# Performance work log

Measured on AMD Instinct MI355X. Metric: run time of the kernel, lower is better.

## Reference

```python
import jax, jax.numpy as jnp
import numpy as np

NUM_GROUPS = 32
NUM_HEAD_CH = 64
EPS = 1e-5


def setup_inputs() -> dict:
    key = jax.random.key(0)
    k1, k2, k3 = jax.random.split(key, 3)
    B, C, H, W = 16, 512, 32, 32
    return {
        "x": jax.random.normal(k1, (B, C, H, W), dtype=jnp.float32),
        "norm_w": jnp.ones((C,), dtype=jnp.float32),
        "norm_b": jnp.zeros((C,), dtype=jnp.float32),
        "qkv_w": jax.random.normal(k2, (3 * C, C), dtype=jnp.float32) * 0.02,
        "qkv_b": jnp.zeros((3 * C,), dtype=jnp.float32),
        "proj_w": jax.random.normal(k3, (C, C), dtype=jnp.float32) * 0.02,
        "proj_b": jnp.zeros((C,), dtype=jnp.float32),
    }


def _group_norm(x, w, b):
    # x: [B, C, T]
    B, C, T = x.shape
    g = x.reshape(B, NUM_GROUPS, C // NUM_GROUPS, T)
    mean = g.mean(axis=(2, 3), keepdims=True)
    var = g.var(axis=(2, 3), keepdims=True)
    g = (g - mean) * jax.lax.rsqrt(var + EPS)
    return g.reshape(B, C, T) * w[None, :, None] + b[None, :, None]


def reference(x, norm_w, norm_b, qkv_w, qkv_b, proj_w, proj_b):
    B, C, Hs, Ws = x.shape
    T = Hs * Ws
    xr = x.reshape(B, C, T)
    xn = _group_norm(xr, norm_w, norm_b)
    # 1x1 conv == matmul over channel dim
    qkv = jnp.einsum('oc,bct->bot', qkv_w, xn) + qkv_b[None, :, None]  # [B, 3C, T]
    q, k, v = jnp.split(qkv, 3, axis=1)
    nH = C // NUM_HEAD_CH
    ch = NUM_HEAD_CH
    q = q.reshape(B * nH, ch, T)
    k = k.reshape(B * nH, ch, T)
    v = v.reshape(B * nH, ch, T)
    scale = 1.0 / np.sqrt(np.sqrt(ch)).astype(np.float32)
    # [BH, T, S] score matrix, softmax in float32 (matches torch .float())
    weight = jnp.einsum('bct,bcs->bts', q * scale, k * scale)
    weight = jax.nn.softmax(weight.astype(jnp.float32), axis=-1).astype(weight.dtype)
    a = jnp.einsum('bts,bcs->bct', weight, v).reshape(B, C, T)
    h = jnp.einsum('oc,bct->bot', proj_w, a) + proj_b[None, :, None]
    return (xr + h).reshape(B, C, Hs, Ws)
```

## Files before the change

### kernel.cpp

```cpp
#include <hip/hip_runtime.h>
#include <hip/hip_bf16.h>


typedef __bf16 bf16x8 __attribute__((ext_vector_type(8)));
typedef __bf16 bf16x4 __attribute__((ext_vector_type(4)));
typedef float f32x4 __attribute__((ext_vector_type(4)));

#define MFMA16(a, b, c) __builtin_amdgcn_mfma_f32_16x16x32_bf16((a), (b), (c), 0, 0, 0)

typedef const __attribute__((address_space(1))) unsigned int* gptr_t;
typedef __attribute__((address_space(3))) unsigned int* lptr_t;

__device__ __forceinline__ void gload16(const void* g, void* l) {
  __builtin_amdgcn_global_load_lds((gptr_t)g, (lptr_t)l, 16, 0, 0);
}

__global__ __launch_bounds__(256) void cvt_bf16(const float* __restrict__ src,
                                                __hip_bfloat16* __restrict__ dst,
                                                int n4) {
  int i = blockIdx.x * 256 + threadIdx.x;
  if (i >= n4) return;
  float4 v = ((const float4*)src)[i];
  union { __hip_bfloat16 h[4]; uint2 u; } pk;
  pk.h[0] = __float2bfloat16(v.x);
  pk.h[1] = __float2bfloat16(v.y);
  pk.h[2] = __float2bfloat16(v.z);
  pk.h[3] = __float2bfloat16(v.w);
  *(uint2*)(dst + (size_t)i * 4) = pk.u;
}

__global__ __launch_bounds__(256) void gn_kernel(const float* __restrict__ x,
                                                 const float* __restrict__ nw,
                                                 const float* __restrict__ nb,
                                                 __hip_bfloat16* __restrict__ xnt) {
  const int blk = blockIdx.x;
  const int bb = blk >> 5, g = blk & 31;
  const int tid = threadIdx.x;
  const float4* xg = (const float4*)(x + ((size_t)bb * 512 + g * 16) * 1024);

  float4 vals[16];
  float s = 0.f, ss = 0.f;
#pragma unroll
  for (int k = 0; k < 16; ++k) {
    float4 v = xg[tid + 256 * k];
    vals[k] = v;
    s += v.x + v.y + v.z + v.w;
    ss += v.x * v.x + v.y * v.y + v.z * v.z + v.w * v.w;
  }
#pragma unroll
  for (int off = 1; off < 64; off <<= 1) {
    s += __shfl_xor(s, off, 64);
    ss += __shfl_xor(ss, off, 64);
  }
  __shared__ float red[8];
  const int wid = tid >> 6, lane = tid & 63;
  if (lane == 0) { red[wid] = s; red[wid + 4] = ss; }
  __syncthreads();
  s = red[0] + red[1] + red[2] + red[3];
  ss = red[4] + red[5] + red[6] + red[7];
  const float mean = s * (1.f / 16384.f);
  const float var = ss * (1.f / 16384.f) - mean * mean;
  const float rstd = rsqrtf(var + 1e-5f);

  float aa[16], cc[16];
#pragma unroll
  for (int k = 0; k < 16; ++k) {
    float w = nw[g * 16 + k];
    float b = nb[g * 16 + k];
    aa[k] = rstd * w;
    cc[k] = b - mean * aa[k];
  }
#pragma unroll
  for (int j = 0; j < 4; ++j) {
    union { __hip_bfloat16 h[16]; uint4 u[2]; } row;
#pragma unroll
    for (int k = 0; k < 16; ++k) {
      float v = ((const float*)&vals[k])[j];
      row.h[k] = __float2bfloat16(v * aa[k] + cc[k]);
    }
    size_t idx = ((size_t)bb * 1024 + 4 * tid + j) * 512 + g * 16;
    *(uint4*)(xnt + idx) = row.u[0];
    *(uint4*)(xnt + idx + 8) = row.u[1];
  }
}

template <int EPI>
__global__ __launch_bounds__(256) void gemm_bt(const __hip_bfloat16* __restrict__ A,
                                               const __hip_bfloat16* __restrict__ Bt,
                                               const float* __restrict__ bias,
                                               __hip_bfloat16* __restrict__ oq,
                                               __hip_bfloat16* __restrict__ ok,
                                               __hip_bfloat16* __restrict__ ov,
                                               const float* __restrict__ xres,
                                               float* __restrict__ of) {
  __shared__ __hip_bfloat16 Alds[128 * 64];
  __shared__ __hip_bfloat16 Blds[128 * 64];
  const int tid = threadIdx.x;
  const int wid = tid >> 6, lane = tid & 63;
  const int g = lane >> 4, tl = lane & 15;
  const int wr = wid >> 1, wc = wid & 1;
  const int id = blockIdx.y * 128 + blockIdx.x;
  const int w = id >> 3;
  const int m0 = (w >> 4) * 128;
  const int n0 = (((id & 7) << 4) | (w & 15)) * 128;

  f32x4 acc[4][4];
#pragma unroll
  for (int i = 0; i < 4; ++i)
#pragma unroll
    for (int j = 0; j < 4; ++j) acc[i][j] = (f32x4){0.f, 0.f, 0.f, 0.f};

  for (int kt = 0; kt < 8; ++kt) {
    const int k0 = kt * 64;
    __syncthreads();
#pragma unroll
    for (int qq = 0; qq < 4; ++qq) {
      const int r = qq * 32 + (tid >> 3);
      const int ko = (tid & 7) * 8;
      gload16(A + (size_t)(m0 + r) * 512 + k0 + ko,
              (char*)Alds + (qq * 2048 + wid * 512) * 2);
      gload16(Bt + (size_t)(n0 + r) * 512 + k0 + ko,
              (char*)Blds + (qq * 2048 + wid * 512) * 2);
    }
    __syncthreads();
#pragma unroll
    for (int kk = 0; kk < 2; ++kk) {
      bf16x8 af[4], bfr[4];
#pragma unroll
      for (int mi = 0; mi < 4; ++mi)
        af[mi] = *(const bf16x8*)(Alds + (wr * 64 + mi * 16 + tl) * 64 + kk * 32 + g * 8);
#pragma unroll
      for (int ni = 0; ni < 4; ++ni)
        bfr[ni] = *(const bf16x8*)(Blds + (wc * 64 + ni * 16 + tl) * 64 + kk * 32 + g * 8);
      __builtin_amdgcn_s_setprio(1);
#pragma unroll
      for (int mi = 0; mi < 4; ++mi)
#pragma unroll
        for (int ni = 0; ni < 4; ++ni)
          acc[mi][ni] = MFMA16(af[mi], bfr[ni], acc[mi][ni]);
      __builtin_amdgcn_s_setprio(0);
    }
  }

  if (EPI == 0) {
    const bool isv = (m0 >= 1024);
    const bool isq = (m0 < 512);
    const float qs = 0.42466090014286f;
#pragma unroll
    for (int mi = 0; mi < 4; ++mi) {
      const int o = m0 + wr * 64 + mi * 16 + g * 4;
      const int och = o & 511, h = och >> 6, cb = och & 63;
#pragma unroll
      for (int ni = 0; ni < 4; ++ni) {
        const int n = n0 + wc * 64 + ni * 16 + tl;
        const int bb2 = n >> 10, t = n & 1023;
        const int bh = bb2 * 8 + h;
        if (!isv) {
          union { __hip_bfloat16 h4[4]; uint2 u; } pk;
#pragma unroll
          for (int r = 0; r < 4; ++r)
            pk.h4[r] = __float2bfloat16((acc[mi][ni][r] + bias[o + r]) * qs);
          __hip_bfloat16* dst = (isq ? oq : ok) + ((size_t)bh * 1024 + t) * 64 + cb;
          *(uint2*)dst = pk.u;
        } else {
#pragma unroll
          for (int r = 0; r < 4; ++r)
            ov[((size_t)bh * 64 + cb + r) * 1024 + t] =
                __float2bfloat16(acc[mi][ni][r] + bias[o + r]);
        }
      }
    }
  } else {
#pragma unroll
    for (int mi = 0; mi < 4; ++mi) {
#pragma unroll
      for (int r = 0; r < 4; ++r) {
        const int o = m0 + wr * 64 + mi * 16 + g * 4 + r;
        const float bv = bias[o];
#pragma unroll
        for (int ni = 0; ni < 4; ++ni) {
          const int n = n0 + wc * 64 + ni * 16 + tl;
          const int bb2 = n >> 10, t = n & 1023;
          const size_t xi = ((size_t)bb2 * 512 + o) * 1024 + t;
          of[xi] = xres[xi] + acc[mi][ni][r] + bv;
        }
      }
    }
  }
}

__global__ __launch_bounds__(512) void attn_kernel(const __hip_bfloat16* __restrict__ qt,
                                                   const __hip_bfloat16* __restrict__ kt,
                                                   const __hip_bfloat16* __restrict__ vv,
                                                   __hip_bfloat16* __restrict__ at) {
  const int blk = blockIdx.x;
  const int xcd = blk & 7;
  const int within = blk >> 3;
  const int tile = within & 3;
  const int bhi = xcd * 16 + (within >> 2);
  const int tid = threadIdx.x;
  const int wid = tid >> 6, lane = tid & 63;
  const int g = lane >> 4, tl = lane & 15;
  const int t0 = tile * 256 + wid * 32;

  const char* qh = (const char*)(qt + (size_t)bhi * 65536);
  const char* kh = (const char*)(kt + (size_t)bhi * 65536);
  const char* vh = (const char*)(vv + (size_t)bhi * 65536);

  __shared__ __hip_bfloat16 Klds[2][4096];
  __shared__ __hip_bfloat16 Vlds[2][4096];
  __shared__ __hip_bfloat16 Plds[8][2048];

  const int swz = (tl & 7) << 4;
  char* Pw = (char*)&Plds[wid][0];

  const int srow = lane >> 3;
  const int ssw = ((lane & 7) * 16) ^ (srow << 4);
  const int rb0 = wid * 8;

  bf16x8 qb[2][2];
#pragma unroll
  for (int qs = 0; qs < 2; ++qs)
#pragma unroll
    for (int h = 0; h < 2; ++h)
      qb[qs][h] = *(const bf16x8*)(qh + (size_t)(t0 + qs * 16 + tl) * 128 + h * 64 + g * 16);

  bf16x8 vones;
#pragma unroll
  for (int i = 0; i < 8; ++i) vones[i] = (__bf16)1.0f;

  f32x4 acc[2][4];
  f32x4 accl[2];
#pragma unroll
  for (int i = 0; i < 2; ++i) {
    accl[i] = (f32x4){0.f, 0.f, 0.f, 0.f};
#pragma unroll
    for (int j = 0; j < 4; ++j) acc[i][j] = (f32x4){0.f, 0.f, 0.f, 0.f};
  }

  {
    const int r = rb0 + srow;
    gload16(kh + (size_t)r * 128 + ssw, (char*)&Klds[0][0] + rb0 * 128);
    gload16(vh + (size_t)r * 2048 + ssw, (char*)&Vlds[0][0] + rb0 * 128);
  }
  __syncthreads();

  int cur = 0;
  for (int sb = 0; sb < 16; ++sb) {
    if (sb < 15) {
      const int s0n = (sb + 1) * 64;
      const int r = rb0 + srow;
      gload16(kh + (size_t)(s0n + r) * 128 + ssw, (char*)&Klds[cur ^ 1][0] + rb0 * 128);
      gload16(vh + (size_t)r * 2048 + s0n * 2 + ssw, (char*)&Vlds[cur ^ 1][0] + rb0 * 128);
    }
    const char* Kb = (const char*)&Klds[cur][0];
    const char* Vb = (const char*)&Vlds[cur][0];

    f32x4 sv[4][2];
#pragma unroll
    for (int st = 0; st < 4; ++st) {
      const int krow = (st * 16 + tl) * 128;
      bf16x8 ka0 = *(const bf16x8*)(Kb + krow + ((g * 16) ^ swz));
      bf16x8 ka1 = *(const bf16x8*)(Kb + krow + ((64 + g * 16) ^ swz));
      __builtin_amdgcn_s_setprio(1);
#pragma unroll
      for (int qs = 0; qs < 2; ++qs) {
        f32x4 z = (f32x4){0.f, 0.f, 0.f, 0.f};
        z = MFMA16(ka0, qb[qs][0], z);
        z = MFMA16(ka1, qb[qs][1], z);
        sv[st][qs] = z;
      }
      __builtin_amdgcn_s_setprio(0);
    }

#pragma unroll
    for (int qs = 0; qs < 2; ++qs) {
#pragma unroll
      for (int st = 0; st < 4; ++st) {
        bf16x4 pu;
#pragma unroll
        for (int r = 0; r < 4; ++r) {
          float p = exp2f(sv[st][qs][r]);
          pu[r] = (__bf16)p;
        }
        *(bf16x4*)(Pw + (qs * 16 + tl) * 128 + ((st * 32 + g * 8) ^ swz)) = pu;
      }
    }

    bf16x8 pa[2][2];
#pragma unroll
    for (int ts = 0; ts < 2; ++ts) {
      const int prow = (ts * 16 + tl) * 128;
      pa[ts][0] = *(const bf16x8*)(Pw + prow + ((g * 16) ^ swz));
      pa[ts][1] = *(const bf16x8*)(Pw + prow + ((64 + g * 16) ^ swz));
    }
    __builtin_amdgcn_s_setprio(1);
#pragma unroll
    for (int ts = 0; ts < 2; ++ts) {
      accl[ts] = MFMA16(pa[ts][0], vones, accl[ts]);
      accl[ts] = MFMA16(pa[ts][1], vones, accl[ts]);
    }
    __builtin_amdgcn_s_setprio(0);
#pragma unroll
    for (int ct = 0; ct < 4; ++ct) {
      const int vrow = (ct * 16 + tl) * 128;
      bf16x8 vb0 = *(const bf16x8*)(Vb + vrow + ((g * 16) ^ swz));
      bf16x8 vb1 = *(const bf16x8*)(Vb + vrow + ((64 + g * 16) ^ swz));
      __builtin_amdgcn_s_setprio(1);
#pragma unroll
      for (int ts = 0; ts < 2; ++ts) {
        acc[ts][ct] = MFMA16(pa[ts][0], vb0, acc[ts][ct]);
        acc[ts][ct] = MFMA16(pa[ts][1], vb1, acc[ts][ct]);
      }
      __builtin_amdgcn_s_setprio(0);
    }
    __syncthreads();
    cur ^= 1;
  }

  const int bb2 = bhi >> 3, hh = bhi & 7;
#pragma unroll
  for (int ts = 0; ts < 2; ++ts) {
#pragma unroll
    for (int r = 0; r < 4; ++r) {
      const float iv = 1.f / accl[ts][r];
      const size_t row = (size_t)bb2 * 1024 + t0 + ts * 16 + g * 4 + r;
#pragma unroll
      for (int ct = 0; ct < 4; ++ct)
        at[row * 512 + hh * 64 + ct * 16 + tl] = __float2bfloat16(acc[ts][ct][r] * iv);
    }
  }
}

extern "C" void kernel_launch(void* const* d_in, const int* in_sizes, int n_in,
                              void* d_out, int out_size, void* d_ws, size_t ws_size,
                              hipStream_t stream) {
  const float* x  = (const float*)d_in[0];
  const float* nw = (const float*)d_in[1];
  const float* nb = (const float*)d_in[2];
  const float* qw = (const float*)d_in[3];
  const float* qb = (const float*)d_in[4];
  const float* pw = (const float*)d_in[5];
  const float* pb = (const float*)d_in[6];
  float* out = (float*)d_out;
  char* ws = (char*)d_ws;

  __hip_bfloat16* xnt = (__hip_bfloat16*)(ws);
  __hip_bfloat16* qtb = (__hip_bfloat16*)(ws + 16777216);
  __hip_bfloat16* ktb = (__hip_bfloat16*)(ws + 33554432);
  __hip_bfloat16* vvb = (__hip_bfloat16*)(ws + 50331648);
  __hip_bfloat16* qwb = (__hip_bfloat16*)(ws + 67108864);
  __hip_bfloat16* pwb = (__hip_bfloat16*)(ws + 68681728);

  cvt_bf16<<<768, 256, 0, stream>>>(qw, qwb, 196608);
  cvt_bf16<<<256, 256, 0, stream>>>(pw, pwb, 65536);
  gn_kernel<<<512, 256, 0, stream>>>(x, nw, nb, xnt);
  gemm_bt<0><<<dim3(128, 12), 256, 0, stream>>>(qwb, xnt, qb, qtb, ktb, vvb,
                                                nullptr, nullptr);
  attn_kernel<<<512, 512, 0, stream>>>(qtb, ktb, vvb, xnt);
  gemm_bt<1><<<dim3(128, 4), 256, 0, stream>>>(pwb, xnt, pb, nullptr, nullptr,
                                               nullptr, x, out);
}
```

Baseline: 149.7 us.

## Widen GEMM tiles to 128x256 with 8 waves, swizzled LDS, XCD-aware block mapping

The projection GEMMs now use 512-thread blocks computing 128x256 output tiles, which doubles B-tile reuse per A load. LDS writes and reads use an XOR swizzle on the column to avoid bank conflicts. Block indices are remapped so that tiles sharing B columns land on the same XCD for L2 reuse. The two weight-conversion launches are merged into one kernel to save a launch. The risks are higher LDS use and lower occupancy with fewer blocks, and the epilogue indexing has to agree with the new wc range.

```diff
diff --git a/kernel.cpp b/kernel.cpp
--- a/kernel.cpp
+++ b/kernel.cpp
@@ -15,11 +15,22 @@
   __builtin_amdgcn_global_load_lds((gptr_t)g, (lptr_t)l, 16, 0, 0);
 }
 
-__global__ __launch_bounds__(256) void cvt_bf16(const float* __restrict__ src,
-                                                __hip_bfloat16* __restrict__ dst,
-                                                int n4) {
+__global__ __launch_bounds__(256) void cvt_bf16_2(const float* __restrict__ s0,
+                                                  __hip_bfloat16* __restrict__ d0,
+                                                  int n0,
+                                                  const float* __restrict__ s1,
+                                                  __hip_bfloat16* __restrict__ d1,
+                                                  int n1) {
   int i = blockIdx.x * 256 + threadIdx.x;
-  if (i >= n4) return;
+  const float* src;
+  __hip_bfloat16* dst;
+  if (i < n0) {
+    src = s0; dst = d0;
+  } else {
+    i -= n0;
+    if (i >= n1) return;
+    src = s1; dst = d1;
+  }
   float4 v = ((const float4*)src)[i];
   union { __hip_bfloat16 h[4]; uint2 u; } pk;
   pk.h[0] = __float2bfloat16(v.x);
@@ -85,7 +96,7 @@
 }
 
 template <int EPI>
-__global__ __launch_bounds__(256) void gemm_bt(const __hip_bfloat16* __restrict__ A,
+__global__ __launch_bounds__(512) void gemm_bt(const __hip_bfloat16* __restrict__ A,
                                                const __hip_bfloat16* __restrict__ Bt,
                                                const float* __restrict__ bias,
                                                __hip_bfloat16* __restrict__ oq,
@@ -94,15 +105,20 @@
                                                const float* __restrict__ xres,
                                                float* __restrict__ of) {
   __shared__ __hip_bfloat16 Alds[128 * 64];
-  __shared__ __hip_bfloat16 Blds[128 * 64];
+  __shared__ __hip_bfloat16 Blds[256 * 64];
   const int tid = threadIdx.x;
   const int wid = tid >> 6, lane = tid & 63;
   const int g = lane >> 4, tl = lane & 15;
-  const int wr = wid >> 1, wc = wid & 1;
-  const int id = blockIdx.y * 128 + blockIdx.x;
-  const int w = id >> 3;
-  const int m0 = (w >> 4) * 128;
-  const int n0 = (((id & 7) << 4) | (w & 15)) * 128;
+  const int wr = wid >> 2, wc = wid & 3;
+  const int NM = (EPI == 0) ? 12 : 4;
+  const int id = blockIdx.x;
+  const int xcd = id & 7, w = id >> 3;
+  const int m0 = (w % NM) * 128;
+  const int n0 = (xcd * 8 + w / NM) * 256;
+
+  const int srow8 = lane >> 3;
+  const int sselem = ((lane & 7) * 8) ^ (srow8 << 3);
+  const int rswz = (tl & 7) << 4;
 
   f32x4 acc[4][4];
 #pragma unroll
@@ -114,24 +130,31 @@
     const int k0 = kt * 64;
     __syncthreads();
 #pragma unroll
-    for (int qq = 0; qq < 4; ++qq) {
-      const int r = qq * 32 + (tid >> 3);
-      const int ko = (tid & 7) * 8;
-      gload16(A + (size_t)(m0 + r) * 512 + k0 + ko,
-              (char*)Alds + (qq * 2048 + wid * 512) * 2);
-      gload16(Bt + (size_t)(n0 + r) * 512 + k0 + ko,
-              (char*)Blds + (qq * 2048 + wid * 512) * 2);
+    for (int q = 0; q < 2; ++q) {
+      const int r = q * 64 + wid * 8 + srow8;
+      gload16(A + (size_t)(m0 + r) * 512 + k0 + sselem,
+              (char*)Alds + q * 8192 + wid * 1024);
+    }
+#pragma unroll
+    for (int q = 0; q < 4; ++q) {
+      const int r = q * 64 + wid * 8 + srow8;
+      gload16(Bt + (size_t)(n0 + r) * 512 + k0 + sselem,
+              (char*)Blds + q * 8192 + wid * 1024);
     }
     __syncthreads();
 #pragma unroll
     for (int kk = 0; kk < 2; ++kk) {
       bf16x8 af[4], bfr[4];
 #pragma unroll
-      for (int mi = 0; mi < 4; ++mi)
-        af[mi] = *(const bf16x8*)(Alds + (wr * 64 + mi * 16 + tl) * 64 + kk * 32 + g * 8);
-#pragma unroll
-      for (int ni = 0; ni < 4; ++ni)
-        bfr[ni] = *(const bf16x8*)(Blds + (wc * 64 + ni * 16 + tl) * 64 + kk * 32 + g * 8);
+      for (int mi = 0; mi < 4; ++mi) {
+        const int row = wr * 64 + mi * 16 + tl;
+        af[mi] = *(const bf16x8*)((char*)Alds + row * 128 + ((kk * 64 + g * 16) ^ rswz));
+      }
+#pragma unroll
+      for (int ni = 0; ni < 4; ++ni) {
+        const int row = wc * 64 + ni * 16 + tl;
+        bfr[ni] = *(const bf16x8*)((char*)Blds + row * 128 + ((kk * 64 + g * 16) ^ rswz));
+      }
       __builtin_amdgcn_s_setprio(1);
 #pragma unroll
       for (int mi = 0; mi < 4; ++mi)
@@ -352,12 +375,11 @@
   __hip_bfloat16* qwb = (__hip_bfloat16*)(ws + 67108864);
   __hip_bfloat16* pwb = (__hip_bfloat16*)(ws + 68681728);
 
-  cvt_bf16<<<768, 256, 0, stream>>>(qw, qwb, 196608);
-  cvt_bf16<<<256, 256, 0, stream>>>(pw, pwb, 65536);
+  cvt_bf16_2<<<1024, 256, 0, stream>>>(qw, qwb, 196608, pw, pwb, 65536);
   gn_kernel<<<512, 256, 0, stream>>>(x, nw, nb, xnt);
-  gemm_bt<0><<<dim3(128, 12), 256, 0, stream>>>(qwb, xnt, qb, qtb, ktb, vvb,
-                                                nullptr, nullptr);
+  gemm_bt<0><<<768, 512, 0, stream>>>(qwb, xnt, qb, qtb, ktb, vvb,
+                                      nullptr, nullptr);
   attn_kernel<<<512, 512, 0, stream>>>(qtb, ktb, vvb, xnt);
-  gemm_bt<1><<<dim3(128, 4), 256, 0, stream>>>(pwb, xnt, pb, nullptr, nullptr,
-                                               nullptr, x, out);
-}
+  gemm_bt<1><<<256, 512, 0, stream>>>(pwb, xnt, pb, nullptr, nullptr,
+                                      nullptr, x, out);
+}
```

New measurement: 141.3 us. 1.06x faster.
